# Kernel optimization log

Hardware: AMD Instinct MI355X
Metric: run time of the kernel (lower is better)

## Reference

```python
import jax, jax.numpy as jnp
import numpy as np

B, C, H, W = 8, 256, 96, 96
GH, GW = 16, 16                # proto_grid
KH, KW = H // GH, W // GW      # avg-pool kernel = stride
P = GH * GW                    # local prototypes per sample
THRESH = 0.95
NORM_EPS = 1e-4


def _safe_norm(x, axis):
    # L2-normalize with norm clamped below at NORM_EPS (matches safe_norm)
    n = jnp.sqrt(jnp.sum(x * x, axis=axis, keepdims=True))
    return x / jnp.maximum(n, NORM_EPS)


def _avg_pool(x):
    # [B, c, H, W] -> [B, c, P] non-overlapping KHxKW average pooling
    b, c = x.shape[:2]
    return x.reshape(b, c, GH, KH, GW, KW).mean(axis=(3, 5)).reshape(b, c, P)


def setup_inputs() -> dict:
    key = jax.random.key(0)
    k1, k2, k3, k4 = jax.random.split(key, 4)
    qry_fts = jax.random.normal(k1, (B, C, H, W), dtype=jnp.float32)
    sup_fts = jax.random.normal(k2, (B, C, H, W), dtype=jnp.float32)
    sup_mask = (jax.random.uniform(k3, (B, 1, H, W)) > 0.02).astype(jnp.float32)
    true_bg_mask = (jax.random.uniform(k4, (B, 1, H, W)) > 0.9).astype(jnp.float32)
    return {"qry_fts": qry_fts, "sup_fts": sup_fts,
            "sup_mask": sup_mask, "true_bg_mask": true_bg_mask}


def reference(qry_fts, sup_fts, sup_mask, true_bg_mask):
    # mode='gridconv+' path, vectorized: ragged prototype selection -> masked softmax
    local_fts = _avg_pool(sup_fts).transpose(0, 2, 1)       # [B, P, C]
    local_mask = _avg_pool(sup_mask)[:, 0, :]               # [B, P]
    local_bg = _avg_pool(true_bg_mask)[:, 0, :]             # [B, P]
    valid = (local_mask > THRESH) & (local_bg < 0.5)        # [B, P] bool

    # global masked-average prototype
    gproto = jnp.sum(sup_fts * sup_mask, axis=(-1, -2)) / (
        jnp.sum(sup_mask, axis=(-1, -2)) + 1e-5)            # [B, C]

    protos = jnp.concatenate([local_fts, gproto[:, None, :]], axis=1)  # [B, P+1, C]
    valid_all = jnp.concatenate(
        [valid, jnp.ones((B, 1), dtype=bool)], axis=1)      # global always valid

    protos_n = _safe_norm(protos, axis=2)                   # [B, P+1, C]
    qry_n = _safe_norm(qry_fts, axis=1)                     # [B, C, H, W]

    # 1x1 conv with prototype weights == batched cosine similarity
    dists = jnp.einsum('bchw,bpc->bphw', qry_n, protos_n)   # [B, P+1, H, W]

    # softmax restricted to valid prototypes (invalid get weight 0)
    logits = jnp.where(valid_all[:, :, None, None], dists, -jnp.inf)
    w = jax.nn.softmax(logits, axis=1)
    pred = jnp.sum(w * dists, axis=1, keepdims=True)        # [B, 1, H, W]
    return pred
```

## Files before the change

### kernel.cpp

```cpp
#include <hip/hip_runtime.h>

#define BB 8
#define CC 256
#define HH 96
#define WW 96
#define HWW (HH*WW)
#define NLOC 256
#define PPAD 257
#define THRESH 0.95f
#define NORM_EPS 1e-4f

typedef __attribute__((ext_vector_type(8))) short bf16x8;
typedef __attribute__((ext_vector_type(4))) float f32x4;

__global__ void k01(const float* __restrict__ sup_fts,
                    const float* __restrict__ sup_mask,
                    const float* __restrict__ true_bg,
                    float* __restrict__ protos,
                    float* __restrict__ validf,
                    float* __restrict__ masksum) {
    __shared__ float red[256];
    int blk = blockIdx.x;
    int t = threadIdx.x;
    if (blk < BB * CC) {
        int b = blk >> 8, c = blk & 255;
        int gy = t >> 4, gx = t & 15;
        const float* fb = sup_fts + ((size_t)b * CC + c) * HWW;
        const float* mb = sup_mask + (size_t)b * HWW;
        int base = gy * 6 * WW + gx * 6;
        float fs = 0.f, fm = 0.f;
        for (int r = 0; r < 6; ++r) {
            const float* rowf = fb + base + r * WW;
            const float* rowm = mb + base + r * WW;
#pragma unroll
            for (int h = 0; h < 3; ++h) {
                float2 v  = *(const float2*)(rowf + 2 * h);
                float2 mk = *(const float2*)(rowm + 2 * h);
                fs += v.x + v.y;
                fm = fmaf(v.x, mk.x, fm);
                fm = fmaf(v.y, mk.y, fm);
            }
        }
        protos[((size_t)b * PPAD + t) * CC + c] = fs * (1.f / 36.f);
        red[t] = fm;
        __syncthreads();
        for (int off = 128; off > 0; off >>= 1) {
            if (t < off) red[t] += red[t + off];
            __syncthreads();
        }
        if (t == 0) protos[((size_t)b * PPAD + 256) * CC + c] = red[0];
    } else {
        int b = blk - BB * CC;
        int gy = t >> 4, gx = t & 15;
        const float* mb = sup_mask + (size_t)b * HWW;
        const float* gb = true_bg  + (size_t)b * HWW;
        int base = gy * 6 * WW + gx * 6;
        float ms = 0.f, bs = 0.f;
        for (int r = 0; r < 6; ++r) {
            const float* rowm = mb + base + r * WW;
            const float* rowg = gb + base + r * WW;
#pragma unroll
            for (int h = 0; h < 3; ++h) {
                float2 mk = *(const float2*)(rowm + 2 * h);
                float2 bg2 = *(const float2*)(rowg + 2 * h);
                ms += mk.x + mk.y;
                bs += bg2.x + bg2.y;
            }
        }
        float mmean = ms * (1.f / 36.f);
        float bmean = bs * (1.f / 36.f);
        validf[b * PPAD + t] = (mmean > THRESH && bmean < 0.5f) ? 1.f : 0.f;
        if (t == 0) validf[b * PPAD + 256] = 1.f;
        red[t] = ms;
        __syncthreads();
        for (int off = 128; off > 0; off >>= 1) {
            if (t < off) red[t] += red[t + off];
            __syncthreads();
        }
        if (t == 0) masksum[b] = red[0];
    }
}

__global__ void k2_norm(float* __restrict__ protos,
                        const float* __restrict__ masksum,
                        unsigned short* __restrict__ Bimg) {
    int bp = blockIdx.x;
    int b = bp / PPAD;
    int p = bp - b * PPAD;
    int t = threadIdx.x;
    float v = protos[((size_t)b * PPAD + p) * CC + t];
    if (p == 256) v = v / (masksum[b] + 1e-5f);
    __shared__ float red[256];
    red[t] = v * v;
    __syncthreads();
    for (int off = 128; off > 0; off >>= 1) {
        if (t < off) red[t] += red[t + off];
        __syncthreads();
    }
    float norm = sqrtf(red[0]);
    float vn = v / fmaxf(norm, NORM_EPS);
    protos[((size_t)b * PPAD + p) * CC + t] = vn;
    if (p < NLOC) {
        unsigned int u = __float_as_uint(vn);
        unsigned short hi = (unsigned short)(u >> 16);
        float lo = vn - __uint_as_float(u & 0xffff0000u);
        unsigned int ul = __float_as_uint(lo);
        unsigned short lob = (unsigned short)((ul + 0x7fffu + ((ul >> 16) & 1u)) >> 16);
        int kc = t >> 5, j = t & 31;
        int ph = p >> 7, pp = p & 127;
        size_t base = ((((size_t)b * 8 + kc) * 2 + ph) * 2) * (128 * 40);
        Bimg[base + (size_t)pp * 40 + j] = hi;
        Bimg[base + 128 * 40 + (size_t)pp * 40 + j] = lob;
    }
}

#define COMPUTE_PH(PH, BUF)                                                        \
    {                                                                              \
        _Pragma("unroll")                                                          \
        for (int ttl = 0; ttl < 8; ++ttl) {                                        \
            int rowoff = (ttl * 16 + n) * 40 + g * 8;                              \
            bf16x8 bh = *(const bf16x8*)&Blds[BUF][rowoff];                        \
            bf16x8 bl = *(const bf16x8*)&Blds[BUF][5120 + rowoff];                 \
            _Pragma("unroll")                                                      \
            for (int sub = 0; sub < 2; ++sub) {                                    \
                acc[sub][(PH)*8 + ttl] = __builtin_amdgcn_mfma_f32_16x16x32_bf16(  \
                    AH[sub], bh, acc[sub][(PH)*8 + ttl], 0, 0, 0);                 \
                acc[sub][(PH)*8 + ttl] = __builtin_amdgcn_mfma_f32_16x16x32_bf16(  \
                    AL[sub], bh, acc[sub][(PH)*8 + ttl], 0, 0, 0);                 \
                acc[sub][(PH)*8 + ttl] = __builtin_amdgcn_mfma_f32_16x16x32_bf16(  \
                    AH[sub], bl, acc[sub][(PH)*8 + ttl], 0, 0, 0);                 \
            }                                                                      \
        }                                                                          \
    }

__global__ __launch_bounds__(256, 2)
void k3_mfma(const float* __restrict__ qry,
             const unsigned short* __restrict__ Bimg,
             const float* __restrict__ protos_n,
             const float* __restrict__ validf,
             float* __restrict__ out) {
    __shared__ alignas(16) unsigned short Blds[2][10240];

    int bid = blockIdx.x;
    int b = bid / (HWW / 128);
    int tile = bid - b * (HWW / 128);
    int t = threadIdx.x;
    int lane = t & 63;
    int w = t >> 6;
    int g = lane >> 4;
    int n = lane & 15;
    int px0 = tile * 128 + w * 32;

    const float* qb = qry + (size_t)b * CC * HWW;
    const float* gp = protos_n + ((size_t)b * PPAD + 256) * CC;
    const unsigned short* Bg = Bimg + (size_t)b * 8 * 2 * 2 * (128 * 40);

    f32x4 acc[2][16];
#pragma unroll
    for (int sub = 0; sub < 2; ++sub)
#pragma unroll
        for (int tt = 0; tt < 16; ++tt)
            acc[sub][tt] = (f32x4){0.f, 0.f, 0.f, 0.f};
    float norm2[2] = {0.f, 0.f};
    float gacc[2] = {0.f, 0.f};
    float q2[2][8];
    float gpv[8];
    bf16x8 AH[2], AL[2];

    auto STAGE = [&](int kc, int ph, int buf) {
        const char* src = (const char*)(Bg + (size_t)(kc * 2 + ph) * (2 * 128 * 40));
        const char* dst = (const char*)(&Blds[buf][0]) + w * 1024;
        int goff = t * 16;
#pragma unroll
        for (int i = 0; i < 5; ++i)
            __builtin_amdgcn_global_load_lds((const void*)(src + i * 4096 + goff),
                                             (void*)(dst + i * 4096), 16, 0, 0);
    };

    auto QLOAD = [&](int kc) {
        int c0 = kc * 32;
#pragma unroll
        for (int sub = 0; sub < 2; ++sub) {
            const float* qcol = qb + (size_t)(c0 + 8 * g) * HWW + (px0 + sub * 16 + n);
#pragma unroll
            for (int j = 0; j < 8; ++j) q2[sub][j] = qcol[(size_t)j * HWW];
        }
#pragma unroll
        for (int j = 0; j < 8; ++j) gpv[j] = gp[c0 + 8 * g + j];
    };

    auto SPLITACC = [&]() {
#pragma unroll
        for (int sub = 0; sub < 2; ++sub) {
            union { bf16x8 v; unsigned int u[4]; } H, L;
#pragma unroll
            for (int jp = 0; jp < 4; ++jp) {
                unsigned int u0 = __float_as_uint(q2[sub][2 * jp]);
                unsigned int u1 = __float_as_uint(q2[sub][2 * jp + 1]);
                H.u[jp] = (u0 >> 16) | (u1 & 0xffff0000u);
                float lo0 = q2[sub][2 * jp]     - __uint_as_float(u0 & 0xffff0000u);
                float lo1 = q2[sub][2 * jp + 1] - __uint_as_float(u1 & 0xffff0000u);
                unsigned int r0 = __float_as_uint(lo0);
                unsigned int r1 = __float_as_uint(lo1);
                r0 = (r0 + 0x7fffu + ((r0 >> 16) & 1u)) >> 16;
                r1 = (r1 + 0x7fffu + ((r1 >> 16) & 1u)) & 0xffff0000u;
                L.u[jp] = r0 | r1;
            }
            AH[sub] = H.v; AL[sub] = L.v;
#pragma unroll
            for (int j = 0; j < 8; ++j) {
                norm2[sub] = fmaf(q2[sub][j], q2[sub][j], norm2[sub]);
                gacc[sub]  = fmaf(q2[sub][j], gpv[j], gacc[sub]);
            }
        }
    };

    STAGE(0, 0, 0);
    QLOAD(0);
    __syncthreads();
    SPLITACC();
    for (int kc = 0; kc < 8; ++kc) {
        STAGE(kc, 1, 1);
        if (kc < 7) QLOAD(kc + 1);
        COMPUTE_PH(0, 0);
        __syncthreads();
        if (kc < 7) STAGE(kc + 1, 0, 0);
        COMPUTE_PH(1, 1);
        __syncthreads();
        if (kc < 7) SPLITACC();
    }

#pragma unroll
    for (int sub = 0; sub < 2; ++sub) {
        norm2[sub] += __shfl_xor(norm2[sub], 16);
        norm2[sub] += __shfl_xor(norm2[sub], 32);
        gacc[sub]  += __shfl_xor(gacc[sub], 16);
        gacc[sub]  += __shfl_xor(gacc[sub], 32);
    }

    float rnorm[2][4], gd[2][4];
#pragma unroll
    for (int sub = 0; sub < 2; ++sub)
#pragma unroll
        for (int r = 0; r < 4; ++r) {
            float n2 = __shfl(norm2[sub], 4 * g + r);
            float rn = 1.f / fmaxf(sqrtf(n2), NORM_EPS);
            rnorm[sub][r] = rn;
            gd[sub][r] = __shfl(gacc[sub], 4 * g + r) * rn;
        }

    float vf[16];
    const float* vb = validf + b * PPAD;
#pragma unroll
    for (int tt = 0; tt < 16; ++tt) vf[tt] = vb[tt * 16 + n];

#pragma unroll
    for (int sub = 0; sub < 2; ++sub) {
        float S[4] = {0.f, 0.f, 0.f, 0.f};
        float NN[4] = {0.f, 0.f, 0.f, 0.f};
#pragma unroll
        for (int tt = 0; tt < 16; ++tt) {
#pragma unroll
            for (int r = 0; r < 4; ++r) {
                float d = acc[sub][tt][r] * rnorm[sub][r];
                float l = (vf[tt] != 0.f) ? d : -1e30f;
                float e = __expf(l - 1.1f);
                S[r] += e;
                NN[r] = fmaf(e, l, NN[r]);
            }
        }
#pragma unroll
        for (int r = 0; r < 4; ++r) {
#pragma unroll
            for (int m = 1; m < 16; m <<= 1) {
                S[r]  += __shfl_xor(S[r], m);
                NN[r] += __shfl_xor(NN[r], m);
            }
            float eg = __expf(gd[sub][r] - 1.1f);
            S[r] += eg;
            NN[r] = fmaf(eg, gd[sub][r], NN[r]);
        }
        if (n < 4) {
            float Ssel = (n == 0) ? S[0] : (n == 1) ? S[1] : (n == 2) ? S[2] : S[3];
            float Nsel = (n == 0) ? NN[0] : (n == 1) ? NN[1] : (n == 2) ? NN[2] : NN[3];
            out[(size_t)b * HWW + px0 + sub * 16 + 4 * g + n] = Nsel / Ssel;
        }
    }
}

extern "C" void kernel_launch(void* const* d_in, const int* in_sizes, int n_in,
                              void* d_out, int out_size, void* d_ws, size_t ws_size,
                              hipStream_t stream) {
    const float* qry = (const float*)d_in[0];
    const float* sup = (const float*)d_in[1];
    const float* msk = (const float*)d_in[2];
    const float* bg  = (const float*)d_in[3];
    float* out = (float*)d_out;

    float* ws = (float*)d_ws;
    float* protos  = ws;
    float* validf  = protos + (size_t)BB * PPAD * CC;
    float* masksum = validf + (size_t)BB * PPAD;
    unsigned short* Bimg = (unsigned short*)(masksum + BB);

    hipLaunchKernelGGL(k01, dim3(BB * CC + BB), dim3(256), 0, stream,
                       sup, msk, bg, protos, validf, masksum);
    hipLaunchKernelGGL(k2_norm, dim3(BB * PPAD), dim3(256), 0, stream, protos, masksum, Bimg);
    hipLaunchKernelGGL(k3_mfma, dim3(BB * (HWW / 128)), dim3(256), 0, stream,
                       qry, Bimg, protos, validf, out);
}
```

Before: 72.50 us.

## Load prototype bf16 tiles straight from global into registers, dropping LDS staging

The k3 kernel no longer stages prototype bf16 hi/lo tiles through double-buffered LDS with block-wide barriers. Each 64-thread, single-wave block now reads the B fragments directly from global memory into registers, double-buffered in software so the next loads overlap the MFMAs. The Bimg layout drops its padded 40-element rows for a dense 32-element stride, and blocks are interleaved across the batch. This removes barriers and LDS traffic, but every wave now fetches the full prototype matrix from cache on its own, which multiplies L2 read traffic roughly by four.

```diff
diff --git a/kernel.cpp b/kernel.cpp
--- a/kernel.cpp
+++ b/kernel.cpp
@@ -107,53 +107,56 @@
         unsigned int ul = __float_as_uint(lo);
         unsigned short lob = (unsigned short)((ul + 0x7fffu + ((ul >> 16) & 1u)) >> 16);
         int kc = t >> 5, j = t & 31;
-        int ph = p >> 7, pp = p & 127;
-        size_t base = ((((size_t)b * 8 + kc) * 2 + ph) * 2) * (128 * 40);
-        Bimg[base + (size_t)pp * 40 + j] = hi;
-        Bimg[base + 128 * 40 + (size_t)pp * 40 + j] = lob;
+        size_t base = ((size_t)(b * 8 + kc) * 2) * 8192;
+        Bimg[base + (size_t)p * 32 + j] = hi;
+        Bimg[base + 8192 + (size_t)p * 32 + j] = lob;
     }
 }
 
-#define COMPUTE_PH(PH, BUF)                                                        \
-    {                                                                              \
-        _Pragma("unroll")                                                          \
-        for (int ttl = 0; ttl < 8; ++ttl) {                                        \
-            int rowoff = (ttl * 16 + n) * 40 + g * 8;                              \
-            bf16x8 bh = *(const bf16x8*)&Blds[BUF][rowoff];                        \
-            bf16x8 bl = *(const bf16x8*)&Blds[BUF][5120 + rowoff];                 \
-            _Pragma("unroll")                                                      \
-            for (int sub = 0; sub < 2; ++sub) {                                    \
-                acc[sub][(PH)*8 + ttl] = __builtin_amdgcn_mfma_f32_16x16x32_bf16(  \
-                    AH[sub], bh, acc[sub][(PH)*8 + ttl], 0, 0, 0);                 \
-                acc[sub][(PH)*8 + ttl] = __builtin_amdgcn_mfma_f32_16x16x32_bf16(  \
-                    AL[sub], bh, acc[sub][(PH)*8 + ttl], 0, 0, 0);                 \
-                acc[sub][(PH)*8 + ttl] = __builtin_amdgcn_mfma_f32_16x16x32_bf16(  \
-                    AH[sub], bl, acc[sub][(PH)*8 + ttl], 0, 0, 0);                 \
-            }                                                                      \
-        }                                                                          \
-    }
-
-__global__ __launch_bounds__(256, 2)
+
+#define LOADB(BHx, BLx, KC, T0)                                              \
+    {                                                                        \
+        const unsigned short* p0 = Bb + (size_t)(KC) * 16384 +               \
+                                   ((T0) * 16 + n) * 32 + g * 8;             \
+        BHx[0] = *(const bf16x8*)(p0);                                       \
+        BHx[1] = *(const bf16x8*)(p0 + 512);                                 \
+        BLx[0] = *(const bf16x8*)(p0 + 8192);                                \
+        BLx[1] = *(const bf16x8*)(p0 + 8704);                                \
+    }
+
+#define MFMA2(BHx, BLx, T0)                                                  \
+    {                                                                        \
+        _Pragma("unroll")                                                    \
+        for (int u = 0; u < 2; ++u) {                                        \
+            _Pragma("unroll")                                                \
+            for (int sub = 0; sub < 2; ++sub) {                              \
+                acc[sub][(T0) + u] = __builtin_amdgcn_mfma_f32_16x16x32_bf16(\
+                    AH[sub], BHx[u], acc[sub][(T0) + u], 0, 0, 0);           \
+                acc[sub][(T0) + u] = __builtin_amdgcn_mfma_f32_16x16x32_bf16(\
+                    AL[sub], BHx[u], acc[sub][(T0) + u], 0, 0, 0);           \
+                acc[sub][(T0) + u] = __builtin_amdgcn_mfma_f32_16x16x32_bf16(\
+                    AH[sub], BLx[u], acc[sub][(T0) + u], 0, 0, 0);           \
+            }                                                                \
+        }                                                                    \
+    }
+
+__global__ __launch_bounds__(64)
 void k3_mfma(const float* __restrict__ qry,
              const unsigned short* __restrict__ Bimg,
              const float* __restrict__ protos_n,
              const float* __restrict__ validf,
              float* __restrict__ out) {
-    __shared__ alignas(16) unsigned short Blds[2][10240];
-
-    int bid = blockIdx.x;
-    int b = bid / (HWW / 128);
-    int tile = bid - b * (HWW / 128);
-    int t = threadIdx.x;
-    int lane = t & 63;
-    int w = t >> 6;
+    int blk = blockIdx.x;
+    int b = blk & 7;
+    int tile = blk >> 3;
+    int lane = threadIdx.x;
     int g = lane >> 4;
     int n = lane & 15;
-    int px0 = tile * 128 + w * 32;
+    int px0 = tile * 32;
 
     const float* qb = qry + (size_t)b * CC * HWW;
     const float* gp = protos_n + ((size_t)b * PPAD + 256) * CC;
-    const unsigned short* Bg = Bimg + (size_t)b * 8 * 2 * 2 * (128 * 40);
+    const unsigned short* Bb = Bimg + (size_t)b * 8 * 2 * 8192;
 
     f32x4 acc[2][16];
 #pragma unroll
@@ -163,43 +166,34 @@
             acc[sub][tt] = (f32x4){0.f, 0.f, 0.f, 0.f};
     float norm2[2] = {0.f, 0.f};
     float gacc[2] = {0.f, 0.f};
-    float q2[2][8];
-    float gpv[8];
+    float qnext[2][8];
+    float gpvn[8];
     bf16x8 AH[2], AL[2];
-
-    auto STAGE = [&](int kc, int ph, int buf) {
-        const char* src = (const char*)(Bg + (size_t)(kc * 2 + ph) * (2 * 128 * 40));
-        const char* dst = (const char*)(&Blds[buf][0]) + w * 1024;
-        int goff = t * 16;
-#pragma unroll
-        for (int i = 0; i < 5; ++i)
-            __builtin_amdgcn_global_load_lds((const void*)(src + i * 4096 + goff),
-                                             (void*)(dst + i * 4096), 16, 0, 0);
-    };
-
-    auto QLOAD = [&](int kc) {
+    bf16x8 BH0[2], BL0[2], BH1[2], BL1[2];
+
+    auto QLOADN = [&](int kc) {
         int c0 = kc * 32;
 #pragma unroll
         for (int sub = 0; sub < 2; ++sub) {
             const float* qcol = qb + (size_t)(c0 + 8 * g) * HWW + (px0 + sub * 16 + n);
 #pragma unroll
-            for (int j = 0; j < 8; ++j) q2[sub][j] = qcol[(size_t)j * HWW];
-        }
-#pragma unroll
-        for (int j = 0; j < 8; ++j) gpv[j] = gp[c0 + 8 * g + j];
+            for (int j = 0; j < 8; ++j) qnext[sub][j] = qcol[(size_t)j * HWW];
+        }
+#pragma unroll
+        for (int j = 0; j < 8; ++j) gpvn[j] = gp[c0 + 8 * g + j];
     };
 
-    auto SPLITACC = [&]() {
+    auto SPLITN = [&]() {
 #pragma unroll
         for (int sub = 0; sub < 2; ++sub) {
             union { bf16x8 v; unsigned int u[4]; } H, L;
 #pragma unroll
             for (int jp = 0; jp < 4; ++jp) {
-                unsigned int u0 = __float_as_uint(q2[sub][2 * jp]);
-                unsigned int u1 = __float_as_uint(q2[sub][2 * jp + 1]);
+                unsigned int u0 = __float_as_uint(qnext[sub][2 * jp]);
+                unsigned int u1 = __float_as_uint(qnext[sub][2 * jp + 1]);
                 H.u[jp] = (u0 >> 16) | (u1 & 0xffff0000u);
-                float lo0 = q2[sub][2 * jp]     - __uint_as_float(u0 & 0xffff0000u);
-                float lo1 = q2[sub][2 * jp + 1] - __uint_as_float(u1 & 0xffff0000u);
+                float lo0 = qnext[sub][2 * jp]     - __uint_as_float(u0 & 0xffff0000u);
+                float lo1 = qnext[sub][2 * jp + 1] - __uint_as_float(u1 & 0xffff0000u);
                 unsigned int r0 = __float_as_uint(lo0);
                 unsigned int r1 = __float_as_uint(lo1);
                 r0 = (r0 + 0x7fffu + ((r0 >> 16) & 1u)) >> 16;
@@ -209,25 +203,35 @@
             AH[sub] = H.v; AL[sub] = L.v;
 #pragma unroll
             for (int j = 0; j < 8; ++j) {
-                norm2[sub] = fmaf(q2[sub][j], q2[sub][j], norm2[sub]);
-                gacc[sub]  = fmaf(q2[sub][j], gpv[j], gacc[sub]);
+                norm2[sub] = fmaf(qnext[sub][j], qnext[sub][j], norm2[sub]);
+                gacc[sub]  = fmaf(qnext[sub][j], gpvn[j], gacc[sub]);
             }
         }
     };
 
-    STAGE(0, 0, 0);
-    QLOAD(0);
-    __syncthreads();
-    SPLITACC();
+    QLOADN(0);
+    LOADB(BH0, BL0, 0, 0);
+    SPLITN();
+
     for (int kc = 0; kc < 8; ++kc) {
-        STAGE(kc, 1, 1);
-        if (kc < 7) QLOAD(kc + 1);
-        COMPUTE_PH(0, 0);
-        __syncthreads();
-        if (kc < 7) STAGE(kc + 1, 0, 0);
-        COMPUTE_PH(1, 1);
-        __syncthreads();
-        if (kc < 7) SPLITACC();
+        LOADB(BH1, BL1, kc, 2);
+        if (kc < 7) QLOADN(kc + 1);
+        MFMA2(BH0, BL0, 0);
+        LOADB(BH0, BL0, kc, 4);
+        MFMA2(BH1, BL1, 2);
+        LOADB(BH1, BL1, kc, 6);
+        MFMA2(BH0, BL0, 4);
+        LOADB(BH0, BL0, kc, 8);
+        MFMA2(BH1, BL1, 6);
+        LOADB(BH1, BL1, kc, 10);
+        MFMA2(BH0, BL0, 8);
+        LOADB(BH0, BL0, kc, 12);
+        MFMA2(BH1, BL1, 10);
+        LOADB(BH1, BL1, kc, 14);
+        MFMA2(BH0, BL0, 12);
+        if (kc < 7) LOADB(BH0, BL0, kc + 1, 0);
+        MFMA2(BH1, BL1, 14);
+        if (kc < 7) SPLITN();
     }
 
 #pragma unroll
@@ -306,6 +310,6 @@
     hipLaunchKernelGGL(k01, dim3(BB * CC + BB), dim3(256), 0, stream,
                        sup, msk, bg, protos, validf, masksum);
     hipLaunchKernelGGL(k2_norm, dim3(BB * PPAD), dim3(256), 0, stream, protos, masksum, Bimg);
-    hipLaunchKernelGGL(k3_mfma, dim3(BB * (HWW / 128)), dim3(256), 0, stream,
+    hipLaunchKernelGGL(k3_mfma, dim3(BB * (HWW / 32)), dim3(64), 0, stream,
                        qry, Bimg, protos, validf, out);
 }
```

Measured after the change: 90.81 us. 25.3% more time.

## Restructure MFMA kernel to split prototypes across waves with shared query tile

Applied to the files above, without the earlier changes.

Reworks the main similarity kernel so each 512-thread block handles 64 pixels. Each of the 8 waves owns 32 prototypes and keeps its bf16 hi/lo prototype fragments in registers, loaded straight from global memory. Query features are loaded cooperatively, split into bf16 hi/lo once, and shared through double-buffered LDS. The masked-softmax partial sums and the query norms are reduced across waves through shared memory. The goals are more blocks and better occupancy, and no redundant per-wave query splitting. The cost is extra LDS traffic, more barriers and a cross-wave reduction step.

```diff
diff --git a/kernel.cpp b/kernel.cpp
--- a/kernel.cpp
+++ b/kernel.cpp
@@ -107,185 +107,171 @@
         unsigned int ul = __float_as_uint(lo);
         unsigned short lob = (unsigned short)((ul + 0x7fffu + ((ul >> 16) & 1u)) >> 16);
         int kc = t >> 5, j = t & 31;
-        int ph = p >> 7, pp = p & 127;
-        size_t base = ((((size_t)b * 8 + kc) * 2 + ph) * 2) * (128 * 40);
-        Bimg[base + (size_t)pp * 40 + j] = hi;
-        Bimg[base + 128 * 40 + (size_t)pp * 40 + j] = lob;
-    }
-}
-
-#define COMPUTE_PH(PH, BUF)                                                        \
-    {                                                                              \
-        _Pragma("unroll")                                                          \
-        for (int ttl = 0; ttl < 8; ++ttl) {                                        \
-            int rowoff = (ttl * 16 + n) * 40 + g * 8;                              \
-            bf16x8 bh = *(const bf16x8*)&Blds[BUF][rowoff];                        \
-            bf16x8 bl = *(const bf16x8*)&Blds[BUF][5120 + rowoff];                 \
-            _Pragma("unroll")                                                      \
-            for (int sub = 0; sub < 2; ++sub) {                                    \
-                acc[sub][(PH)*8 + ttl] = __builtin_amdgcn_mfma_f32_16x16x32_bf16(  \
-                    AH[sub], bh, acc[sub][(PH)*8 + ttl], 0, 0, 0);                 \
-                acc[sub][(PH)*8 + ttl] = __builtin_amdgcn_mfma_f32_16x16x32_bf16(  \
-                    AL[sub], bh, acc[sub][(PH)*8 + ttl], 0, 0, 0);                 \
-                acc[sub][(PH)*8 + ttl] = __builtin_amdgcn_mfma_f32_16x16x32_bf16(  \
-                    AH[sub], bl, acc[sub][(PH)*8 + ttl], 0, 0, 0);                 \
-            }                                                                      \
-        }                                                                          \
-    }
-
-__global__ __launch_bounds__(256, 2)
+        size_t base = ((size_t)(b * 8 + kc) * 2) * 8192;
+        Bimg[base + (size_t)p * 32 + j] = hi;
+        Bimg[base + 8192 + (size_t)p * 32 + j] = lob;
+    }
+}
+
+__global__ __launch_bounds__(512, 4)
 void k3_mfma(const float* __restrict__ qry,
              const unsigned short* __restrict__ Bimg,
              const float* __restrict__ protos_n,
              const float* __restrict__ validf,
              float* __restrict__ out) {
-    __shared__ alignas(16) unsigned short Blds[2][10240];
+    __shared__ unsigned short Albuf[2][2][2560];
+    __shared__ float nrm_l[8][64], gac_l[8][64];
+    __shared__ float S_l[8][64], N_l[8][64];
+    __shared__ float rn_s[64], gd_s[64];
 
     int bid = blockIdx.x;
-    int b = bid / (HWW / 128);
-    int tile = bid - b * (HWW / 128);
+    int b = bid / 144;
+    int tile = bid - b * 144;
     int t = threadIdx.x;
     int lane = t & 63;
     int w = t >> 6;
     int g = lane >> 4;
     int n = lane & 15;
-    int px0 = tile * 128 + w * 32;
+    int px0 = tile * 64;
+
+    int spx = t & 63;
+    int k4 = (t >> 6) * 4;
 
     const float* qb = qry + (size_t)b * CC * HWW;
     const float* gp = protos_n + ((size_t)b * PPAD + 256) * CC;
-    const unsigned short* Bg = Bimg + (size_t)b * 8 * 2 * 2 * (128 * 40);
-
-    f32x4 acc[2][16];
-#pragma unroll
-    for (int sub = 0; sub < 2; ++sub)
-#pragma unroll
-        for (int tt = 0; tt < 16; ++tt)
-            acc[sub][tt] = (f32x4){0.f, 0.f, 0.f, 0.f};
-    float norm2[2] = {0.f, 0.f};
-    float gacc[2] = {0.f, 0.f};
-    float q2[2][8];
-    float gpv[8];
-    bf16x8 AH[2], AL[2];
-
-    auto STAGE = [&](int kc, int ph, int buf) {
-        const char* src = (const char*)(Bg + (size_t)(kc * 2 + ph) * (2 * 128 * 40));
-        const char* dst = (const char*)(&Blds[buf][0]) + w * 1024;
-        int goff = t * 16;
-#pragma unroll
-        for (int i = 0; i < 5; ++i)
-            __builtin_amdgcn_global_load_lds((const void*)(src + i * 4096 + goff),
-                                             (void*)(dst + i * 4096), 16, 0, 0);
-    };
-
-    auto QLOAD = [&](int kc) {
-        int c0 = kc * 32;
-#pragma unroll
-        for (int sub = 0; sub < 2; ++sub) {
-            const float* qcol = qb + (size_t)(c0 + 8 * g) * HWW + (px0 + sub * 16 + n);
-#pragma unroll
-            for (int j = 0; j < 8; ++j) q2[sub][j] = qcol[(size_t)j * HWW];
-        }
-#pragma unroll
-        for (int j = 0; j < 8; ++j) gpv[j] = gp[c0 + 8 * g + j];
-    };
-
-    auto SPLITACC = [&]() {
-#pragma unroll
-        for (int sub = 0; sub < 2; ++sub) {
-            union { bf16x8 v; unsigned int u[4]; } H, L;
-#pragma unroll
-            for (int jp = 0; jp < 4; ++jp) {
-                unsigned int u0 = __float_as_uint(q2[sub][2 * jp]);
-                unsigned int u1 = __float_as_uint(q2[sub][2 * jp + 1]);
-                H.u[jp] = (u0 >> 16) | (u1 & 0xffff0000u);
-                float lo0 = q2[sub][2 * jp]     - __uint_as_float(u0 & 0xffff0000u);
-                float lo1 = q2[sub][2 * jp + 1] - __uint_as_float(u1 & 0xffff0000u);
-                unsigned int r0 = __float_as_uint(lo0);
-                unsigned int r1 = __float_as_uint(lo1);
-                r0 = (r0 + 0x7fffu + ((r0 >> 16) & 1u)) >> 16;
-                r1 = (r1 + 0x7fffu + ((r1 >> 16) & 1u)) & 0xffff0000u;
-                L.u[jp] = r0 | r1;
-            }
-            AH[sub] = H.v; AL[sub] = L.v;
-#pragma unroll
-            for (int j = 0; j < 8; ++j) {
-                norm2[sub] = fmaf(q2[sub][j], q2[sub][j], norm2[sub]);
-                gacc[sub]  = fmaf(q2[sub][j], gpv[j], gacc[sub]);
-            }
-        }
-    };
-
-    STAGE(0, 0, 0);
-    QLOAD(0);
-    __syncthreads();
-    SPLITACC();
+    const unsigned short* Bb = Bimg + (size_t)b * 8 * 2 * 8192;
+
+    f32x4 acc[4][2];
+#pragma unroll
+    for (int s = 0; s < 4; ++s)
+#pragma unroll
+        for (int c = 0; c < 2; ++c) acc[s][c] = (f32x4){0.f, 0.f, 0.f, 0.f};
+
+    float nrm = 0.f, gac = 0.f;
+    float qs[2][4], gpv[2][4];
+    bf16x8 BH[2][2], BL[2][2];
+
+#define QLOADN(KC, QP)                                                        \
+    {                                                                         \
+        int c0 = (KC) * 32 + k4;                                              \
+        _Pragma("unroll")                                                     \
+        for (int j = 0; j < 4; ++j) {                                         \
+            qs[QP][j]  = qb[(size_t)(c0 + j) * HWW + px0 + spx];              \
+            gpv[QP][j] = gp[c0 + j];                                          \
+        }                                                                     \
+    }
+
+#define LOADB(KC, BUF)                                                        \
+    {                                                                         \
+        _Pragma("unroll")                                                     \
+        for (int ct = 0; ct < 2; ++ct) {                                      \
+            const unsigned short* p0 = Bb + (size_t)(KC) * 16384 +            \
+                                       (w * 32 + ct * 16 + n) * 32 + g * 8;   \
+            BH[BUF][ct] = *(const bf16x8*)(p0);                               \
+            BL[BUF][ct] = *(const bf16x8*)(p0 + 8192);                        \
+        }                                                                     \
+    }
+
+#define SPLITW(QP, BUF)                                                       \
+    {                                                                         \
+        unsigned int hh[4], ll[4];                                            \
+        _Pragma("unroll")                                                     \
+        for (int j = 0; j < 4; ++j) {                                         \
+            float qv = qs[QP][j];                                             \
+            unsigned int u = __float_as_uint(qv);                             \
+            hh[j] = u >> 16;                                                  \
+            float lof = qv - __uint_as_float(u & 0xffff0000u);                \
+            unsigned int ul = __float_as_uint(lof);                           \
+            ll[j] = (ul + 0x7fffu + ((ul >> 16) & 1u)) >> 16;                 \
+            nrm = fmaf(qv, qv, nrm);                                          \
+            gac = fmaf(qv, gpv[QP][j], gac);                                  \
+        }                                                                     \
+        uint2 Hp, Lp;                                                         \
+        Hp.x = hh[0] | (hh[1] << 16); Hp.y = hh[2] | (hh[3] << 16);           \
+        Lp.x = ll[0] | (ll[1] << 16); Lp.y = ll[2] | (ll[3] << 16);           \
+        *(uint2*)&Albuf[BUF][0][spx * 40 + k4] = Hp;                          \
+        *(uint2*)&Albuf[BUF][1][spx * 40 + k4] = Lp;                          \
+    }
+
+    LOADB(0, 0);
+    QLOADN(0, 0);
+    LOADB(1, 1);
+    QLOADN(1, 1);
+    SPLITW(0, 0);
+    __syncthreads();
+
+#pragma unroll
     for (int kc = 0; kc < 8; ++kc) {
-        STAGE(kc, 1, 1);
-        if (kc < 7) QLOAD(kc + 1);
-        COMPUTE_PH(0, 0);
-        __syncthreads();
-        if (kc < 7) STAGE(kc + 1, 0, 0);
-        COMPUTE_PH(1, 1);
-        __syncthreads();
-        if (kc < 7) SPLITACC();
-    }
-
-#pragma unroll
-    for (int sub = 0; sub < 2; ++sub) {
-        norm2[sub] += __shfl_xor(norm2[sub], 16);
-        norm2[sub] += __shfl_xor(norm2[sub], 32);
-        gacc[sub]  += __shfl_xor(gacc[sub], 16);
-        gacc[sub]  += __shfl_xor(gacc[sub], 32);
-    }
-
-    float rnorm[2][4], gd[2][4];
-#pragma unroll
-    for (int sub = 0; sub < 2; ++sub)
+        if (kc < 6) QLOADN(kc + 2, kc & 1);
+#pragma unroll
+        for (int sub = 0; sub < 4; ++sub) {
+            bf16x8 AHf = *(const bf16x8*)&Albuf[kc & 1][0][(sub * 16 + n) * 40 + g * 8];
+            bf16x8 ALf = *(const bf16x8*)&Albuf[kc & 1][1][(sub * 16 + n) * 40 + g * 8];
+#pragma unroll
+            for (int ct = 0; ct < 2; ++ct) {
+                acc[sub][ct] = __builtin_amdgcn_mfma_f32_16x16x32_bf16(AHf, BH[kc & 1][ct], acc[sub][ct], 0, 0, 0);
+                acc[sub][ct] = __builtin_amdgcn_mfma_f32_16x16x32_bf16(ALf, BH[kc & 1][ct], acc[sub][ct], 0, 0, 0);
+                acc[sub][ct] = __builtin_amdgcn_mfma_f32_16x16x32_bf16(AHf, BL[kc & 1][ct], acc[sub][ct], 0, 0, 0);
+            }
+        }
+        if (kc < 6) LOADB(kc + 2, kc & 1);
+        if (kc < 7) {
+            SPLITW((kc + 1) & 1, (kc + 1) & 1);
+            __syncthreads();
+        }
+    }
+
+    nrm_l[w][spx] = nrm;
+    gac_l[w][spx] = gac;
+    __syncthreads();
+    if (t < 64) {
+        float n2 = 0.f, gs = 0.f;
+#pragma unroll
+        for (int i = 0; i < 8; ++i) { n2 += nrm_l[i][t]; gs += gac_l[i][t]; }
+        float rn = 1.f / fmaxf(sqrtf(n2), NORM_EPS);
+        rn_s[t] = rn;
+        gd_s[t] = gs * rn;
+    }
+    __syncthreads();
+
+    float vf0 = validf[b * PPAD + w * 32 + n];
+    float vf1 = validf[b * PPAD + w * 32 + 16 + n];
+#pragma unroll
+    for (int sub = 0; sub < 4; ++sub) {
 #pragma unroll
         for (int r = 0; r < 4; ++r) {
-            float n2 = __shfl(norm2[sub], 4 * g + r);
-            float rn = 1.f / fmaxf(sqrtf(n2), NORM_EPS);
-            rnorm[sub][r] = rn;
-            gd[sub][r] = __shfl(gacc[sub], 4 * g + r) * rn;
-        }
-
-    float vf[16];
-    const float* vb = validf + b * PPAD;
-#pragma unroll
-    for (int tt = 0; tt < 16; ++tt) vf[tt] = vb[tt * 16 + n];
-
-#pragma unroll
-    for (int sub = 0; sub < 2; ++sub) {
-        float S[4] = {0.f, 0.f, 0.f, 0.f};
-        float NN[4] = {0.f, 0.f, 0.f, 0.f};
-#pragma unroll
-        for (int tt = 0; tt < 16; ++tt) {
-#pragma unroll
-            for (int r = 0; r < 4; ++r) {
-                float d = acc[sub][tt][r] * rnorm[sub][r];
-                float l = (vf[tt] != 0.f) ? d : -1e30f;
-                float e = __expf(l - 1.1f);
-                S[r] += e;
-                NN[r] = fmaf(e, l, NN[r]);
-            }
-        }
-#pragma unroll
-        for (int r = 0; r < 4; ++r) {
+            int px = sub * 16 + 4 * g + r;
+            float rnv = rn_s[px];
+            float d0 = acc[sub][0][r] * rnv;
+            float d1 = acc[sub][1][r] * rnv;
+            float l0 = (vf0 != 0.f) ? d0 : -1e30f;
+            float l1 = (vf1 != 0.f) ? d1 : -1e30f;
+            float e0 = __expf(l0 - 1.1f);
+            float e1 = __expf(l1 - 1.1f);
+            float s = e0 + e1;
+            float nn = fmaf(e0, l0, e1 * l1);
 #pragma unroll
             for (int m = 1; m < 16; m <<= 1) {
-                S[r]  += __shfl_xor(S[r], m);
-                NN[r] += __shfl_xor(NN[r], m);
-            }
-            float eg = __expf(gd[sub][r] - 1.1f);
-            S[r] += eg;
-            NN[r] = fmaf(eg, gd[sub][r], NN[r]);
-        }
-        if (n < 4) {
-            float Ssel = (n == 0) ? S[0] : (n == 1) ? S[1] : (n == 2) ? S[2] : S[3];
-            float Nsel = (n == 0) ? NN[0] : (n == 1) ? NN[1] : (n == 2) ? NN[2] : NN[3];
-            out[(size_t)b * HWW + px0 + sub * 16 + 4 * g + n] = Nsel / Ssel;
-        }
-    }
+                s  += __shfl_xor(s, m);
+                nn += __shfl_xor(nn, m);
+            }
+            if (n == 0) { S_l[w][px] = s; N_l[w][px] = nn; }
+        }
+    }
+    __syncthreads();
+
+    if (t < 64) {
+        float gdv = gd_s[t];
+        float eg = __expf(gdv - 1.1f);
+        float S = eg, N = eg * gdv;
+#pragma unroll
+        for (int i = 0; i < 8; ++i) { S += S_l[i][t]; N += N_l[i][t]; }
+        out[(size_t)b * HWW + px0 + t] = N / S;
+    }
+
+#undef QLOADN
+#undef LOADB
+#undef SPLITW
 }
 
 extern "C" void kernel_launch(void* const* d_in, const int* in_sizes, int n_in,
@@ -306,6 +292,6 @@
     hipLaunchKernelGGL(k01, dim3(BB * CC + BB), dim3(256), 0, stream,
                        sup, msk, bg, protos, validf, masksum);
     hipLaunchKernelGGL(k2_norm, dim3(BB * PPAD), dim3(256), 0, stream, protos, masksum, Bimg);
-    hipLaunchKernelGGL(k3_mfma, dim3(BB * (HWW / 128)), dim3(256), 0, stream,
+    hipLaunchKernelGGL(k3_mfma, dim3(BB * (HWW / 64)), dim3(512), 0, stream,
                        qry, Bimg, protos, validf, out);
 }
```

Measured after the change: 71.59 us. About the same (-1.3%).
